# Optimization experiments

Measured on AMD Instinct MI355X. Metric: run time of the kernel, lower is better.

## Reference

```python
import jax, jax.numpy as jnp
import numpy as np

T, A = 4096, 4          # tokens, atoms per token
N = T * A               # flat atoms
QB, KB = 32, 128        # query block / key window (AF3 atom transformer)
S = N // QB             # number of query subsets
H, DK = 4, 32           # heads, key dim per head
NB = 3                  # transformer blocks
CA, CP, CT = 128, 16, 384

# clipped sliding key window centered on each 32-atom query block
KIDX = jnp.clip(jnp.arange(S)[:, None] * QB - (KB - QB) // 2 + jnp.arange(KB)[None, :], 0, N - 1)

PARAM_SHAPES = [('w_ref_pos', (3, CA)), ('w_ref_mask', (1, CA)), ('w_ref_element', (CA, CA)), ('w_ref_charge', (1, CA)), ('w_ref_atom_name', (256, CA)), ('w_s2p_row', (CA, CP)), ('w_s2p_col', (CA, CP)), ('w_pair_offsets', (3, CP)), ('w_pair_dist', (1, CP)), ('w_pair_mask', (1, CP)), ('w_pair_mlp1', (CP, CP)), ('w_pair_mlp2', (CP, CP)), ('w_pair_mlp3', (CP, CP)), ('w_pair_ln', (CP,)), ('w_pair_logits', (CP, NB * H)), ('aq_lnw', (NB, CA)), ('aq_gw', (NB, CA, CA)), ('aq_gb', (NB, CA)), ('aq_sw', (NB, CA, CA)), ('ak_lnw', (NB, CA)), ('ak_gw', (NB, CA, CA)), ('ak_gb', (NB, CA)), ('ak_sw', (NB, CA, CA)), ('wq', (NB, CA, CA)), ('bq', (NB, CA)), ('wk', (NB, CA, CA)), ('wv', (NB, CA, CA)), ('wg', (NB, CA, CA)), ('azi_w', (NB, CA, CA)), ('azi_cw', (NB, CA, CA)), ('azi_cb', (NB, CA)), ('t_lnw', (NB, CA)), ('t_gw', (NB, CA, CA)), ('t_gb', (NB, CA)), ('t_sw', (NB, CA, CA)), ('glu1', (NB, CA, 2 * CA)), ('glu2', (NB, CA, 2 * CA)), ('t_azi_w', (NB, 2 * CA, CA)), ('t_azi_cw', (NB, CA, CA)), ('t_azi_cb', (NB, CA)), ('w_project', (CA, CT))]


def _ln(x, w=None, eps=1e-5):
    mu = jnp.mean(x, -1, keepdims=True)
    var = jnp.var(x, -1, keepdims=True)
    xn = (x - mu) * jax.lax.rsqrt(var + eps)
    return xn * w if w is not None else xn


def _ada_ln(x, cond, lnw, gw, gb, sw):
    c = _ln(cond, lnw)
    return jax.nn.sigmoid(c @ gw + gb) * _ln(x) + c @ sw


def setup_inputs() -> dict:
    ks = iter(jax.random.split(jax.random.key(0), 64))
    d = {}
    d['positions'] = jax.random.normal(next(ks), (T, A, 3), jnp.float32) * 3.0
    d['mask'] = jnp.ones((T, A), jnp.float32)
    d['element'] = jax.random.randint(next(ks), (T, A), 0, 128, jnp.int32)
    d['charge'] = jax.random.normal(next(ks), (T, A), jnp.float32)
    d['atom_name_chars'] = jax.random.randint(next(ks), (T, A, 4), 0, 64, jnp.int32)
    d['ref_space_uid'] = jax.random.randint(next(ks), (T, A), 0, T, jnp.int32)
    for nm, shp in PARAM_SHAPES:
        if nm.endswith('lnw') or nm == 'w_pair_ln':
            d[nm] = jnp.ones(shp, jnp.float32)
        else:
            d[nm] = jax.random.normal(next(ks), shp, jnp.float32) * 0.02
    return d


def _forward(positions, mask, charge, w_ref_pos, w_ref_mask, w_ref_element, w_ref_charge, w_ref_atom_name, w_s2p_row, w_s2p_col, w_pair_offsets, w_pair_dist, w_pair_mask, w_pair_mlp1, w_pair_mlp2, w_pair_mlp3, w_pair_ln, w_pair_logits, aq_lnw, aq_gw, aq_gb, aq_sw, ak_lnw, ak_gw, ak_gb, ak_sw, wq, bq, wk, wv, wg, azi_w, azi_cw, azi_cb, t_lnw, t_gw, t_gb, t_sw, glu1, glu2, t_azi_w, t_azi_cw, t_azi_cb, w_project, element, atom_name_chars, ref_space_uid):
    dt = positions.dtype
    pos = positions.reshape(N, 3)
    m = mask.reshape(N, 1)
    # per_atom_cond
    el1h = jax.nn.one_hot(element.reshape(N), 128, dtype=dt)
    nm1h = jax.nn.one_hot(atom_name_chars.reshape(N, 4), 64, dtype=dt).reshape(N, 256)
    ch = jnp.arcsinh(charge.reshape(N, 1))
    act = pos @ w_ref_pos + m @ w_ref_mask + el1h @ w_ref_element + ch @ w_ref_charge + nm1h @ w_ref_atom_name
    act = act * m
    qsc = act.reshape(S, QB, CA)  # queries_single_cond
    # pair conditioning
    uid = ref_space_uid.reshape(N)
    q_uid, k_uid = uid.reshape(S, QB), uid[KIDX]
    q_pos, k_pos = pos.reshape(S, QB, 3), pos[KIDX]
    valid = (q_uid[:, :, None] == k_uid[:, None, :]).astype(dt)[..., None]  # [S,QB,KB,1]
    off = q_pos[:, :, None, :] - k_pos[:, None, :, :]  # [S,QB,KB,3]
    pair = (off @ w_pair_offsets) * valid
    sq = jnp.sum(off * off, -1, keepdims=True)
    pair = pair + ((1.0 / (1.0 + sq)) @ w_pair_dist) * valid
    ksc = act[KIDX]  # keys_single_cond [S,KB,CA]
    pair = pair + (jax.nn.relu(qsc) @ w_s2p_row)[:, :, None, :] + (jax.nn.relu(ksc) @ w_s2p_col)[:, None, :, :]
    pair = pair + valid @ w_pair_mask
    t = jax.nn.relu(pair) @ w_pair_mlp1
    t = jax.nn.relu(t) @ w_pair_mlp2
    t = jax.nn.relu(t) @ w_pair_mlp3
    pair = pair + t
    # pair logits for all blocks: [NB, S, H, QB, KB]
    pl = (_ln(pair, w_pair_ln) @ w_pair_logits).reshape(S, QB, KB, NB, H)
    pl = jnp.transpose(pl, (3, 0, 4, 1, 2))
    qact = qsc
    scale = DK ** -0.5
    for i in range(NB):
        kact = qact.reshape(N, CA)[KIDX]
        xq = _ada_ln(qact, qsc, aq_lnw[i], aq_gw[i], aq_gb[i], aq_sw[i])
        xk = _ada_ln(kact, ksc, ak_lnw[i], ak_gw[i], ak_gb[i], ak_sw[i])
        q = (xq @ wq[i] + bq[i]).reshape(S, QB, H, DK)
        k = (xk @ wk[i]).reshape(S, KB, H, DK)
        logits = jnp.einsum('sqhd,skhd->shqk', q * scale, k) + pl[i]
        aw = jax.nn.softmax(logits, axis=-1)
        v = (xk @ wv[i]).reshape(S, KB, H, DK)
        o = jnp.einsum('shqk,skhd->sqhd', aw, v).reshape(S, QB, CA)
        o = o * jax.nn.sigmoid(xq @ wg[i])
        o = (o @ azi_w[i]) * jax.nn.sigmoid(qsc @ azi_cw[i] + azi_cb[i])  # AdaptiveZeroInit
        qact = qact + o
        xt = _ada_ln(qact, qsc, t_lnw[i], t_gw[i], t_gb[i], t_sw[i])
        xt = jax.nn.silu(xt @ glu1[i]) * (xt @ glu2[i])  # SwiGLU
        xt = (xt @ t_azi_w[i]) * jax.nn.sigmoid(qsc @ t_azi_cw[i] + t_azi_cb[i])
        qact = qact + xt
    tok = jax.nn.relu(qact.reshape(T, A, CA) @ w_project)
    mm = mask[..., None]
    token_act = jnp.sum(tok * mm, -2) / jnp.maximum(jnp.sum(mm, -2), 1e-10)
    return token_act, qact, qsc, pair


def reference(positions, mask, element, charge, atom_name_chars, ref_space_uid, w_ref_pos, w_ref_mask, w_ref_element, w_ref_charge, w_ref_atom_name, w_s2p_row, w_s2p_col, w_pair_offsets, w_pair_dist, w_pair_mask, w_pair_mlp1, w_pair_mlp2, w_pair_mlp3, w_pair_ln, w_pair_logits, aq_lnw, aq_gw, aq_gb, aq_sw, ak_lnw, ak_gw, ak_gb, ak_sw, wq, bq, wk, wv, wg, azi_w, azi_cw, azi_cb, t_lnw, t_gw, t_gb, t_sw, glu1, glu2, t_azi_w, t_azi_cw, t_azi_cb, w_project):
    return _forward(positions, mask, charge, w_ref_pos, w_ref_mask, w_ref_element, w_ref_charge, w_ref_atom_name, w_s2p_row, w_s2p_col, w_pair_offsets, w_pair_dist, w_pair_mask, w_pair_mlp1, w_pair_mlp2, w_pair_mlp3, w_pair_ln, w_pair_logits, aq_lnw, aq_gw, aq_gb, aq_sw, ak_lnw, ak_gw, ak_gb, ak_sw, wq, bq, wk, wv, wg, azi_w, azi_cw, azi_cb, t_lnw, t_gw, t_gb, t_sw, glu1, glu2, t_azi_w, t_azi_cw, t_azi_cb, w_project, element, atom_name_chars, ref_space_uid)
```

## Files before the change

### kernel.cpp

```cpp
#include <hip/hip_runtime.h>
#include <math.h>

#define TT 4096
#define AA 4
#define NN 16384
#define QBQ 32
#define KBK 128
#define SS 512
#define HH 4
#define DKD 32
#define CAC 128
#define CPC 16
#define CTC 384

typedef __attribute__((ext_vector_type(8))) short bf16x8;
typedef __attribute__((ext_vector_type(4))) short s16x4;
typedef __attribute__((ext_vector_type(4))) float f32x4;

__device__ __forceinline__ float sig_(float x) { return 1.0f / (1.0f + __expf(-x)); }
__device__ __forceinline__ short f2bf(float f) {
    unsigned u = __float_as_uint(f);
    unsigned r = (u + 0x7FFFu + ((u >> 16) & 1u)) >> 16;
    return (short)r;
}
__device__ __forceinline__ float b2f(short s) {
    return __uint_as_float(((unsigned)(unsigned short)s) << 16);
}

struct PEnt { const float* src; const float* rs; short* dst; int K; int NC; };
struct PTab { PEnt e[49]; };

__global__ __launch_bounds__(256) void k_prep(PTab tab)
{
    const PEnt e = tab.e[blockIdx.y];
    const int ntx = e.NC >> 5, nty = e.K >> 5, nt = ntx * nty;
    __shared__ float sm[32][33];
    const int lx = threadIdx.x & 31, ly = threadIdx.x >> 5;
    for (int t = blockIdx.x; t < nt; t += gridDim.x) {
        const int ty = t / ntx, tx = t - ty * ntx;
        #pragma unroll
        for (int j = 0; j < 4; ++j) {
            const int k = ty * 32 + ly + j * 8;
            const int n = tx * 32 + lx;
            float v = e.src[(size_t)k * e.NC + n];
            if (e.rs) v *= e.rs[k];
            sm[ly + j * 8][lx] = v;
        }
        __syncthreads();
        #pragma unroll
        for (int j = 0; j < 4; ++j) {
            const int n = tx * 32 + ly + j * 8;
            const int k = ty * 32 + lx;
            e.dst[(size_t)n * e.K + k] = f2bf(sm[lx][ly + j * 8]);
        }
        __syncthreads();
    }
}

__global__ __launch_bounds__(128) void k_atom_cond(
    const float* __restrict__ pos, const float* __restrict__ msk,
    const int* __restrict__ elem, const float* __restrict__ chg,
    const int* __restrict__ chars,
    const float* __restrict__ w_pos, const float* __restrict__ w_msk,
    const float* __restrict__ w_elem, const float* __restrict__ w_chg,
    const float* __restrict__ w_name,
    const float* __restrict__ w_row, const float* __restrict__ w_col,
    float* __restrict__ qsc, float* __restrict__ qact,
    short* __restrict__ qsc_bf, short* __restrict__ qn_bf,
    float* __restrict__ stats,
    float* __restrict__ rq, float* __restrict__ rk)
{
    const int n = blockIdx.x, c = threadIdx.x;
    const float p0 = pos[n*3+0], p1 = pos[n*3+1], p2 = pos[n*3+2];
    const float m = msk[n];
    const int   el = elem[n];
    const float ach = asinhf(chg[n]);
    const int c0 = chars[n*4+0], c1 = chars[n*4+1], c2 = chars[n*4+2], c3 = chars[n*4+3];

    float a = p0*w_pos[c] + p1*w_pos[CAC+c] + p2*w_pos[2*CAC+c]
            + m*w_msk[c] + w_elem[el*CAC+c] + ach*w_chg[c]
            + w_name[(c0      )*CAC+c] + w_name[( 64+c1)*CAC+c]
            + w_name[(128+c2)*CAC+c] + w_name[(192+c3)*CAC+c];
    a *= m;

    const size_t base = (size_t)n*CAC + c;
    qsc[base] = a; qact[base] = a; qsc_bf[base] = f2bf(a);

    __shared__ float red[128];
    __shared__ float sh[128];
    red[c] = a; __syncthreads();
    for (int off = 64; off > 0; off >>= 1) { if (c < off) red[c] += red[c+off]; __syncthreads(); }
    const float mu = red[0] * (1.0f/128.0f);
    __syncthreads();
    const float d = a - mu;
    red[c] = d*d; __syncthreads();
    for (int off = 64; off > 0; off >>= 1) { if (c < off) red[c] += red[c+off]; __syncthreads(); }
    const float var = red[0] * (1.0f/128.0f);
    const float rs = rsqrtf(var + 1e-5f);
    qn_bf[base] = f2bf(d * rs);
    if (c == 0) { stats[2*n] = mu; stats[2*n+1] = rs; }
    __syncthreads();
    sh[c] = fmaxf(a, 0.0f);
    __syncthreads();
    if (c < 32) {
        const float* w = (c < 16) ? w_row : w_col;
        const int cc = c & 15;
        float acc = 0.0f;
        #pragma unroll 8
        for (int r = 0; r < 128; ++r) acc += sh[r] * w[r*CPC + cc];
        if (c < 16) rq[(size_t)n*CPC + cc] = acc;
        else        rk[(size_t)n*CPC + cc] = acc;
    }
}

__global__ __launch_bounds__(256) void k_pair(
    const float* __restrict__ pos, const int* __restrict__ uid,
    const float* __restrict__ rq, const float* __restrict__ rk,
    const float* __restrict__ w_ofs, const float* __restrict__ w_dist,
    const float* __restrict__ w_pm,
    const float* __restrict__ mlp1, const float* __restrict__ mlp2,
    const float* __restrict__ mlp3,
    const float* __restrict__ wln, const float* __restrict__ wpl,
    float* __restrict__ pair, short* __restrict__ plb)
{
    __shared__ float sm1[256], sm2[256], sm3[256], sofs[48], sdist[16], smask[16];
    __shared__ float swln[16], swpl[192];
    const int tid = threadIdx.x;
    sm1[tid] = mlp1[tid]; sm2[tid] = mlp2[tid]; sm3[tid] = mlp3[tid];
    if (tid < 48) sofs[tid] = w_ofs[tid];
    if (tid < 16) { sdist[tid] = w_dist[tid]; smask[tid] = w_pm[tid]; swln[tid] = wln[tid]; }
    if (tid < 192) swpl[tid] = wpl[tid];
    __syncthreads();

    const int gid = blockIdx.x*256 + tid;
    const int s = gid >> 12;
    const int rem = gid & 4095;
    const int q = rem >> 7, kk = rem & 127;
    const int n = s*QBQ + q;
    int kidx = s*QBQ - 48 + kk; kidx = max(0, min(NN-1, kidx));

    const float v = (uid[n] == uid[kidx]) ? 1.0f : 0.0f;
    const float o0 = pos[n*3+0]-pos[kidx*3+0];
    const float o1 = pos[n*3+1]-pos[kidx*3+1];
    const float o2 = pos[n*3+2]-pos[kidx*3+2];
    const float sq = o0*o0 + o1*o1 + o2*o2;
    const float inv = 1.0f/(1.0f + sq);

    const float* rqp = rq + (size_t)n*CPC;
    const float* rkp = rk + (size_t)kidx*CPC;

    float p[16], t1[16], t2[16];
    #pragma unroll
    for (int j = 0; j < 16; ++j)
        p[j] = v*(o0*sofs[j] + o1*sofs[16+j] + o2*sofs[32+j] + inv*sdist[j] + smask[j])
             + rqp[j] + rkp[j];
    #pragma unroll
    for (int j = 0; j < 16; ++j) {
        float acc = 0.0f;
        #pragma unroll
        for (int r = 0; r < 16; ++r) acc += fmaxf(p[r], 0.0f) * sm1[r*16+j];
        t1[j] = acc;
    }
    #pragma unroll
    for (int j = 0; j < 16; ++j) {
        float acc = 0.0f;
        #pragma unroll
        for (int r = 0; r < 16; ++r) acc += fmaxf(t1[r], 0.0f) * sm2[r*16+j];
        t2[j] = acc;
    }
    #pragma unroll
    for (int j = 0; j < 16; ++j) {
        float acc = 0.0f;
        #pragma unroll
        for (int r = 0; r < 16; ++r) acc += fmaxf(t2[r], 0.0f) * sm3[r*16+j];
        t1[j] = p[j] + acc;
    }
    float* op = pair + (size_t)gid*CPC;
    #pragma unroll
    for (int j = 0; j < 4; ++j)
        *(float4*)(op + j*4) = make_float4(t1[j*4], t1[j*4+1], t1[j*4+2], t1[j*4+3]);

    float sm = 0.0f;
    #pragma unroll
    for (int j = 0; j < 16; ++j) sm += t1[j];
    const float mu = sm * (1.0f/16.0f);
    float vq = 0.0f;
    #pragma unroll
    for (int j = 0; j < 16; ++j) { const float dd = t1[j]-mu; vq += dd*dd; }
    const float rs = rsqrtf(vq*(1.0f/16.0f) + 1e-5f);
    float xn[16];
    #pragma unroll
    for (int j = 0; j < 16; ++j) xn[j] = (t1[j]-mu)*rs*swln[j];
    #pragma unroll
    for (int i = 0; i < 3; ++i) {
        #pragma unroll
        for (int h = 0; h < 4; ++h) {
            float acc = 0.0f;
            #pragma unroll
            for (int j = 0; j < 16; ++j) acc += xn[j] * swpl[j*12 + i*4 + h];
            plb[((((size_t)i*SS + s)*HH + h)*QBQ + q)*KBK + kk] = f2bf(acc);
        }
    }
}

struct FJob {
    const void* A; const void* A2;
    const float* stats; const short* G; const short* S;
    const short* Bt; const float* bias;
    float* outF; short* outB;
    const short* gate; float* resid; float* ostats;
    int K; int ostride; int amode; int emode;
};
struct FJobs { FJob j[8]; };

__global__ __launch_bounds__(256) void k_mmf(FJobs jobs)
{
    __shared__ short As[128*64];
    __shared__ short Bs[128*64];
    const FJob J = jobs.j[blockIdx.y];
    const int tid = threadIdx.x;
    const int wave = tid >> 6, lane = tid & 63;
    const int l15 = lane & 15, l4 = lane >> 4;
    const int row0 = blockIdx.x * 128;
    const int K = J.K;

    f32x4 acc[2][8];
    #pragma unroll
    for (int m = 0; m < 2; ++m)
        #pragma unroll
        for (int n = 0; n < 8; ++n) acc[m][n] = (f32x4){0.f,0.f,0.f,0.f};

    for (int k0 = 0; k0 < K; k0 += 64) {
        #pragma unroll
        for (int j = 0; j < 4; ++j) {
            const int u = tid + j*256;
            const int r = u >> 3, ug = u & 7;
            const int row = row0 + r;
            const size_t ao = (size_t)row*K + k0 + ug*8;
            bf16x8 av;
            if (J.amode == 0) {
                av = *(const bf16x8*)((const short*)J.A + ao);
            } else if (J.amode == 1) {
                const float* Af = (const float*)J.A;
                const float4 a0 = *(const float4*)(Af + ao);
                const float4 a1 = *(const float4*)(Af + ao + 4);
                const float mu = J.stats[2*row], rs = J.stats[2*row+1];
                const s16x4 g0 = *(const s16x4*)(J.G + ao), g1 = *(const s16x4*)(J.G + ao + 4);
                const s16x4 s0 = *(const s16x4*)(J.S + ao), s1 = *(const s16x4*)(J.S + ao + 4);
                const float x[8] = {a0.x,a0.y,a0.z,a0.w,a1.x,a1.y,a1.z,a1.w};
                #pragma unroll
                for (int t = 0; t < 4; ++t) {
                    av[t]   = f2bf(b2f(g0[t])*((x[t]  -mu)*rs) + b2f(s0[t]));
                    av[t+4] = f2bf(b2f(g1[t])*((x[t+4]-mu)*rs) + b2f(s1[t]));
                }
            } else if (J.amode == 2) {
                const float* Ao = (const float*)J.A;
                const float* Ag = (const float*)J.A2;
                const float4 oa = *(const float4*)(Ao + ao);
                const float4 ob = *(const float4*)(Ao + ao + 4);
                const float4 ga = *(const float4*)(Ag + ao);
                const float4 gb = *(const float4*)(Ag + ao + 4);
                av[0]=f2bf(oa.x*ga.x); av[1]=f2bf(oa.y*ga.y); av[2]=f2bf(oa.z*ga.z); av[3]=f2bf(oa.w*ga.w);
                av[4]=f2bf(ob.x*gb.x); av[5]=f2bf(ob.y*gb.y); av[6]=f2bf(ob.z*gb.z); av[7]=f2bf(ob.w*gb.w);
            } else {
                const float* Af = (const float*)J.A;
                const float4 a0 = *(const float4*)(Af + ao);
                const float4 a1 = *(const float4*)(Af + ao + 4);
                av[0]=f2bf(a0.x); av[1]=f2bf(a0.y); av[2]=f2bf(a0.z); av[3]=f2bf(a0.w);
                av[4]=f2bf(a1.x); av[5]=f2bf(a1.y); av[6]=f2bf(a1.z); av[7]=f2bf(a1.w);
            }
            *(bf16x8*)&As[r*64 + ((ug ^ (r & 7)) * 8)] = av;
            const bf16x8 bv = *(const bf16x8*)(J.Bt + (size_t)r*K + k0 + ug*8);
            *(bf16x8*)&Bs[r*64 + ((ug ^ (r & 7)) * 8)] = bv;
        }
        __syncthreads();
        #pragma unroll
        for (int ks = 0; ks < 2; ++ks) {
            bf16x8 af[2], bfr[8];
            #pragma unroll
            for (int m = 0; m < 2; ++m) {
                const int r = wave*32 + m*16 + l15;
                af[m] = *(const bf16x8*)&As[r*64 + (((ks*4 + l4) ^ (r & 7)) * 8)];
            }
            #pragma unroll
            for (int n = 0; n < 8; ++n) {
                const int c = n*16 + l15;
                bfr[n] = *(const bf16x8*)&Bs[c*64 + (((ks*4 + l4) ^ (c & 7)) * 8)];
            }
            #pragma unroll
            for (int m = 0; m < 2; ++m)
                #pragma unroll
                for (int n = 0; n < 8; ++n)
                    acc[m][n] = __builtin_amdgcn_mfma_f32_16x16x32_bf16(af[m], bfr[n], acc[m][n], 0, 0, 0);
        }
        __syncthreads();
    }

    if (J.emode == 3) {
        #pragma unroll
        for (int m = 0; m < 2; ++m) {
            #pragma unroll
            for (int reg = 0; reg < 4; ++reg) {
                const int row = row0 + wave*32 + m*16 + l4*4 + reg;
                float s = 0.0f, q = 0.0f;
                #pragma unroll
                for (int n = 0; n < 8; ++n) {
                    const int col = n*16 + l15;
                    const size_t off = (size_t)row*CAC + col;
                    const float v = J.resid[off] + acc[m][n][reg] * b2f(J.gate[off]);
                    J.resid[off] = v;
                    s += v; q += v*v;
                }
                #pragma unroll
                for (int msk = 1; msk < 16; msk <<= 1) {
                    s += __shfl_xor(s, msk, 64);
                    q += __shfl_xor(q, msk, 64);
                }
                if (l15 == 0) {
                    const float mu = s * (1.0f/128.0f);
                    const float var = q * (1.0f/128.0f) - mu*mu;
                    J.ostats[2*row]   = mu;
                    J.ostats[2*row+1] = rsqrtf(var + 1e-5f);
                }
            }
        }
    } else {
        float bval[8];
        #pragma unroll
        for (int n = 0; n < 8; ++n) bval[n] = 0.0f;
        if (J.bias) {
            #pragma unroll
            for (int n = 0; n < 8; ++n) bval[n] = J.bias[n*16 + l15];
        }
        const int epi = J.emode;
        #pragma unroll
        for (int m = 0; m < 2; ++m) {
            #pragma unroll
            for (int n = 0; n < 8; ++n) {
                const int col = n*16 + l15;
                #pragma unroll
                for (int reg = 0; reg < 4; ++reg) {
                    const int row = row0 + wave*32 + m*16 + l4*4 + reg;
                    float v = acc[m][n][reg] + bval[n];
                    if (epi == 1) v = sig_(v);
                    if (epi == 2) v = fmaxf(v, 0.0f);
                    if (J.outB) J.outB[(size_t)row*J.ostride + col] = f2bf(v);
                    else        J.outF[(size_t)row*J.ostride + col] = v;
                }
            }
        }
    }
}

__global__ __launch_bounds__(256) void k_mm_glu(
    const float* __restrict__ qact, const float* __restrict__ stats,
    const short* __restrict__ Gt, const short* __restrict__ St,
    const short* __restrict__ B1t, const short* __restrict__ B2t,
    short* __restrict__ out)
{
    __shared__ short As[128*64];
    __shared__ short B1s[64*64];
    __shared__ short B2s[64*64];
    const int tid = threadIdx.x;
    const int wave = tid >> 6, lane = tid & 63;
    const int l15 = lane & 15, l4 = lane >> 4;
    const int row0 = blockIdx.x * 128;
    const int col0 = blockIdx.y * 64;

    f32x4 acc1[2][4], acc2[2][4];
    #pragma unroll
    for (int m = 0; m < 2; ++m)
        #pragma unroll
        for (int n = 0; n < 4; ++n) {
            acc1[m][n] = (f32x4){0.f,0.f,0.f,0.f};
            acc2[m][n] = (f32x4){0.f,0.f,0.f,0.f};
        }

    for (int k0 = 0; k0 < 128; k0 += 64) {
        #pragma unroll
        for (int j = 0; j < 4; ++j) {
            const int u = tid + j*256;
            const int r = u >> 3, ug = u & 7;
            const int row = row0 + r;
            const size_t ao = (size_t)row*CAC + k0 + ug*8;
            const float4 a0 = *(const float4*)(qact + ao);
            const float4 a1 = *(const float4*)(qact + ao + 4);
            const float mu = stats[2*row], rs = stats[2*row+1];
            const s16x4 g0 = *(const s16x4*)(Gt + ao), g1 = *(const s16x4*)(Gt + ao + 4);
            const s16x4 s0 = *(const s16x4*)(St + ao), s1 = *(const s16x4*)(St + ao + 4);
            const float x[8] = {a0.x,a0.y,a0.z,a0.w,a1.x,a1.y,a1.z,a1.w};
            bf16x8 av;
            #pragma unroll
            for (int t = 0; t < 4; ++t) {
                av[t]   = f2bf(b2f(g0[t])*((x[t]  -mu)*rs) + b2f(s0[t]));
                av[t+4] = f2bf(b2f(g1[t])*((x[t+4]-mu)*rs) + b2f(s1[t]));
            }
            *(bf16x8*)&As[r*64 + ((ug ^ (r & 7)) * 8)] = av;
        }
        #pragma unroll
        for (int j = 0; j < 2; ++j) {
            const int u = tid + j*256;
            const int r = u >> 3, ug = u & 7;
            const bf16x8 b1 = *(const bf16x8*)(B1t + (size_t)(col0 + r)*128 + k0 + ug*8);
            *(bf16x8*)&B1s[r*64 + ((ug ^ (r & 7)) * 8)] = b1;
            const bf16x8 b2 = *(const bf16x8*)(B2t + (size_t)(col0 + r)*128 + k0 + ug*8);
            *(bf16x8*)&B2s[r*64 + ((ug ^ (r & 7)) * 8)] = b2;
        }
        __syncthreads();
        #pragma unroll
        for (int ks = 0; ks < 2; ++ks) {
            bf16x8 af[2], bq1[4], bq2[4];
            #pragma unroll
            for (int m = 0; m < 2; ++m) {
                const int r = wave*32 + m*16 + l15;
                af[m] = *(const bf16x8*)&As[r*64 + (((ks*4 + l4) ^ (r & 7)) * 8)];
            }
            #pragma unroll
            for (int n = 0; n < 4; ++n) {
                const int c = n*16 + l15;
                bq1[n] = *(const bf16x8*)&B1s[c*64 + (((ks*4 + l4) ^ (c & 7)) * 8)];
                bq2[n] = *(const bf16x8*)&B2s[c*64 + (((ks*4 + l4) ^ (c & 7)) * 8)];
            }
            #pragma unroll
            for (int m = 0; m < 2; ++m)
                #pragma unroll
                for (int n = 0; n < 4; ++n) {
                    acc1[m][n] = __builtin_amdgcn_mfma_f32_16x16x32_bf16(af[m], bq1[n], acc1[m][n], 0, 0, 0);
                    acc2[m][n] = __builtin_amdgcn_mfma_f32_16x16x32_bf16(af[m], bq2[n], acc2[m][n], 0, 0, 0);
                }
        }
        __syncthreads();
    }

    #pragma unroll
    for (int m = 0; m < 2; ++m)
        #pragma unroll
        for (int n = 0; n < 4; ++n) {
            const int col = col0 + n*16 + l15;
            #pragma unroll
            for (int reg = 0; reg < 4; ++reg) {
                const int row = row0 + wave*32 + m*16 + l4*4 + reg;
                const float a1 = acc1[m][n][reg];
                const float h = a1 * sig_(a1) * acc2[m][n][reg];
                out[(size_t)row*256 + col] = f2bf(h);
            }
        }
}

__global__ __launch_bounds__(512) void k_attn2(
    const float* __restrict__ qh, const float* __restrict__ kh,
    const float* __restrict__ vh, const short* __restrict__ pls,
    float* __restrict__ oh)
{
    __shared__ float sm_m[256], sm_l[256], sm_acc[256*17];
    const int s = blockIdx.x, tid = threadIdx.x;
    const int kh2 = tid >> 8;
    const int h = (tid >> 6) & 3;
    const int q = (tid >> 1) & 31;
    const int dh = tid & 1;
    const int n0 = s*QBQ;
    const int kbase = n0 - 48 + kh2*64;
    const float SCALE = 0.17677669529663687f;

    float qr[32];
    {
        const float* qp = qh + (size_t)(n0+q)*CAC + h*DKD;
        #pragma unroll
        for (int j = 0; j < 8; ++j) {
            const float4 v4 = *(const float4*)(qp + j*4);
            qr[j*4]=v4.x*SCALE; qr[j*4+1]=v4.y*SCALE; qr[j*4+2]=v4.z*SCALE; qr[j*4+3]=v4.w*SCALE;
        }
    }
    const short* plp = pls + (((size_t)s*HH + h)*QBQ + q)*KBK + kh2*64;

    float m = -1e30f, l = 0.0f;
    float acc[16];
    #pragma unroll
    for (int j = 0; j < 16; ++j) acc[j] = 0.0f;

    for (int kb4 = 0; kb4 < 16; ++kb4) {
        const s16x4 p4 = *(const s16x4*)(plp + kb4*4);
        float pv[4];
        #pragma unroll
        for (int j = 0; j < 4; ++j) pv[j] = b2f(p4[j]);
        #pragma unroll
        for (int j = 0; j < 4; ++j) {
            const int kb = kb4*4 + j;
            int kidx = kbase + kb; kidx = max(0, min(NN-1, kidx));
            const float* kp = kh + (size_t)kidx*CAC + h*DKD;
            float dot = 0.0f;
            #pragma unroll
            for (int jj = 0; jj < 8; ++jj) {
                const float4 kv = *(const float4*)(kp + jj*4);
                dot += qr[jj*4]*kv.x + qr[jj*4+1]*kv.y + qr[jj*4+2]*kv.z + qr[jj*4+3]*kv.w;
            }
            const float sv = dot + pv[j];
            if (sv > m) {
                const float corr = __expf(m - sv);
                l *= corr;
                #pragma unroll
                for (int d = 0; d < 16; ++d) acc[d] *= corr;
                m = sv;
            }
            const float w = __expf(sv - m);
            l += w;
            const float* vp = vh + (size_t)kidx*CAC + h*DKD + dh*16;
            #pragma unroll
            for (int jj = 0; jj < 4; ++jj) {
                const float4 vv = *(const float4*)(vp + jj*4);
                acc[jj*4]   = fmaf(w, vv.x, acc[jj*4]);
                acc[jj*4+1] = fmaf(w, vv.y, acc[jj*4+1]);
                acc[jj*4+2] = fmaf(w, vv.z, acc[jj*4+2]);
                acc[jj*4+3] = fmaf(w, vv.w, acc[jj*4+3]);
            }
        }
    }

    const int part = tid & 255;
    if (kh2 == 1) {
        sm_m[part] = m; sm_l[part] = l;
        #pragma unroll
        for (int j = 0; j < 16; ++j) sm_acc[part*17 + j] = acc[j];
    }
    __syncthreads();
    if (kh2 == 0) {
        const float m2 = sm_m[part], l2 = sm_l[part];
        const float mm = fmaxf(m, m2);
        const float c1 = __expf(m - mm), c2 = __expf(m2 - mm);
        const float inv = 1.0f / (l*c1 + l2*c2);
        float* op = oh + (size_t)(n0+q)*CAC + h*DKD + dh*16;
        #pragma unroll
        for (int jj = 0; jj < 4; ++jj) {
            float o0 = (acc[jj*4  ]*c1 + sm_acc[part*17+jj*4  ]*c2) * inv;
            float o1 = (acc[jj*4+1]*c1 + sm_acc[part*17+jj*4+1]*c2) * inv;
            float o2 = (acc[jj*4+2]*c1 + sm_acc[part*17+jj*4+2]*c2) * inv;
            float o3 = (acc[jj*4+3]*c1 + sm_acc[part*17+jj*4+3]*c2) * inv;
            *(float4*)op = make_float4(o0,o1,o2,o3);
            op += 4;
        }
    }
}

__global__ __launch_bounds__(256) void k_token_reduce(
    const float* __restrict__ tok, const float* __restrict__ msk, float* __restrict__ out)
{
    const int gid = blockIdx.x*256 + threadIdx.x;
    const int t = gid / CTC, c = gid - t*CTC;
    float num = 0.0f, den = 0.0f;
    #pragma unroll
    for (int a = 0; a < AA; ++a) {
        const float mv = msk[t*AA + a];
        num += tok[(size_t)(t*AA+a)*CTC + c] * mv;
        den += mv;
    }
    out[gid] = num / fmaxf(den, 1e-10f);
}

static inline FJob fj0() { FJob j{}; return j; }

extern "C" void kernel_launch(void* const* d_in, const int* in_sizes, int n_in,
                              void* d_out, int out_size, void* d_ws, size_t ws_size,
                              hipStream_t stream)
{
    const float* positions = (const float*)d_in[0];
    const float* maskp     = (const float*)d_in[1];
    const int*   element   = (const int*  )d_in[2];
    const float* charge    = (const float*)d_in[3];
    const int*   chars     = (const int*  )d_in[4];
    const int*   uid       = (const int*  )d_in[5];
    const float* w_ref_pos      = (const float*)d_in[6];
    const float* w_ref_mask     = (const float*)d_in[7];
    const float* w_ref_element  = (const float*)d_in[8];
    const float* w_ref_charge   = (const float*)d_in[9];
    const float* w_ref_atom_name= (const float*)d_in[10];
    const float* w_s2p_row      = (const float*)d_in[11];
    const float* w_s2p_col      = (const float*)d_in[12];
    const float* w_pair_offsets = (const float*)d_in[13];
    const float* w_pair_dist    = (const float*)d_in[14];
    const float* w_pair_mask    = (const float*)d_in[15];
    const float* w_pair_mlp1    = (const float*)d_in[16];
    const float* w_pair_mlp2    = (const float*)d_in[17];
    const float* w_pair_mlp3    = (const float*)d_in[18];
    const float* w_pair_ln      = (const float*)d_in[19];
    const float* w_pair_logits  = (const float*)d_in[20];
    const float* aq_lnw = (const float*)d_in[21];
    const float* aq_gw  = (const float*)d_in[22];
    const float* aq_gb  = (const float*)d_in[23];
    const float* aq_sw  = (const float*)d_in[24];
    const float* ak_lnw = (const float*)d_in[25];
    const float* ak_gw  = (const float*)d_in[26];
    const float* ak_gb  = (const float*)d_in[27];
    const float* ak_sw  = (const float*)d_in[28];
    const float* wq     = (const float*)d_in[29];
    const float* bq     = (const float*)d_in[30];
    const float* wk     = (const float*)d_in[31];
    const float* wv     = (const float*)d_in[32];
    const float* wg     = (const float*)d_in[33];
    const float* azi_w  = (const float*)d_in[34];
    const float* azi_cw = (const float*)d_in[35];
    const float* azi_cb = (const float*)d_in[36];
    const float* t_lnw  = (const float*)d_in[37];
    const float* t_gw   = (const float*)d_in[38];
    const float* t_gb   = (const float*)d_in[39];
    const float* t_sw   = (const float*)d_in[40];
    const float* glu1   = (const float*)d_in[41];
    const float* glu2   = (const float*)d_in[42];
    const float* t_azi_w  = (const float*)d_in[43];
    const float* t_azi_cw = (const float*)d_in[44];
    const float* t_azi_cb = (const float*)d_in[45];
    const float* w_project= (const float*)d_in[46];

    float* token_o = (float*)d_out;
    float* qact = token_o + 1572864;
    float* qsc  = token_o + 3670016;
    float* pair = token_o + 5767168;

    char* W = (char*)d_ws;
    short* pl_bf   = (short*)(W);
    short* wbf     = (short*)(W + 50331648);
    short* qn_bf   = (short*)(W + 52428800);
    short* qsc_bf  = (short*)(W + 56623104);
    float* stats   = (float*)(W + 60817408);
    short* Gq_bf   = (short*)(W + 60948480);
    short* Sq_bf   = (short*)(W + 65142784);
    short* Gk_bf   = (short*)(W + 69337088);
    short* Sk_bf   = (short*)(W + 73531392);
    short* Gt_bf   = (short*)(W + 77725696);
    short* St_bf   = (short*)(W + 81920000);
    short* Ag_bf   = (short*)(W + 86114304);
    short* Tg_bf   = (short*)(W + 90308608);
    float* w_q     = (float*)(W + 94502912);
    float* w_k     = (float*)(W + 102891520);
    float* w_v     = (float*)(W + 111280128);
    float* w_g     = (float*)(W + 119668736);
    float* w_o     = (float*)(W + 128057344);
    short* hs_bf   = (short*)(W + 136445952);
    float* rq      = (float*)(W + 144834560);
    float* rk      = (float*)(W + 145883136);
    float* tok = w_q;

    (void)in_sizes; (void)n_in; (void)out_size; (void)ws_size;

    const size_t LSTR = 311296;
    const size_t oGQ=0, oSQ=16384, oGK=32768, oSK=49152, oGT=65536, oST=81920,
                 oWQ=98304, oWK=114688, oWV=131072, oWG=147456, oAZ=163840,
                 oACW=180224, oTCW=196608, oG1=212992, oG2=245760, oTAW=278528;
    const size_t oPROJ = 3*LSTR;

    {
        PTab tab{};
        int e = 0;
        for (int i = 0; i < 3; ++i) {
            short* L = wbf + (size_t)i*LSTR;
            const size_t oM = (size_t)i*CAC*CAC, oV = (size_t)i*CAC, oGL = (size_t)i*CAC*2*CAC;
            tab.e[e++] = {aq_gw+oM,  aq_lnw+oV, L+oGQ,  128, 128};
            tab.e[e++] = {aq_sw+oM,  aq_lnw+oV, L+oSQ,  128, 128};
            tab.e[e++] = {ak_gw+oM,  ak_lnw+oV, L+oGK,  128, 128};
            tab.e[e++] = {ak_sw+oM,  ak_lnw+oV, L+oSK,  128, 128};
            tab.e[e++] = {t_gw+oM,   t_lnw+oV,  L+oGT,  128, 128};
            tab.e[e++] = {t_sw+oM,   t_lnw+oV,  L+oST,  128, 128};
            tab.e[e++] = {wq+oM,     nullptr,   L+oWQ,  128, 128};
            tab.e[e++] = {wk+oM,     nullptr,   L+oWK,  128, 128};
            tab.e[e++] = {wv+oM,     nullptr,   L+oWV,  128, 128};
            tab.e[e++] = {wg+oM,     nullptr,   L+oWG,  128, 128};
            tab.e[e++] = {azi_w+oM,  nullptr,   L+oAZ,  128, 128};
            tab.e[e++] = {azi_cw+oM, nullptr,   L+oACW, 128, 128};
            tab.e[e++] = {t_azi_cw+oM,nullptr,  L+oTCW, 128, 128};
            tab.e[e++] = {glu1+oGL,  nullptr,   L+oG1,  128, 256};
            tab.e[e++] = {glu2+oGL,  nullptr,   L+oG2,  128, 256};
            tab.e[e++] = {t_azi_w+oGL,nullptr,  L+oTAW, 256, 128};
        }
        tab.e[e++] = {w_project, nullptr, wbf+oPROJ, 128, 384};
        k_prep<<<dim3(48, 49), 256, 0, stream>>>(tab);
    }

    k_atom_cond<<<NN, 128, 0, stream>>>(positions, maskp, element, charge, chars,
        w_ref_pos, w_ref_mask, w_ref_element, w_ref_charge, w_ref_atom_name,
        w_s2p_row, w_s2p_col, qsc, qact, qsc_bf, qn_bf, stats, rq, rk);

    k_pair<<<(SS*QBQ*KBK)/256, 256, 0, stream>>>(positions, uid, rq, rk,
        w_pair_offsets, w_pair_dist, w_pair_mask, w_pair_mlp1, w_pair_mlp2, w_pair_mlp3,
        w_pair_ln, w_pair_logits, pair, pl_bf);

    for (int i = 0; i < 3; ++i) {
        short* L = wbf + (size_t)i*LSTR;
        const size_t oV = (size_t)i*CAC;

        {
            FJobs js{};
            struct { const short* A; const short* Bt; const float* bias; short* out; int em; } cfg[8] = {
                {qn_bf,  L+oGQ,  aq_gb+oV,    Gq_bf, 1}, {qn_bf,  L+oSQ,  nullptr, Sq_bf, 0},
                {qn_bf,  L+oGK,  ak_gb+oV,    Gk_bf, 1}, {qn_bf,  L+oSK,  nullptr, Sk_bf, 0},
                {qn_bf,  L+oGT,  t_gb+oV,     Gt_bf, 1}, {qn_bf,  L+oST,  nullptr, St_bf, 0},
                {qsc_bf, L+oACW, azi_cb+oV,   Ag_bf, 1}, {qsc_bf, L+oTCW, t_azi_cb+oV, Tg_bf, 1}};
            for (int jn = 0; jn < 8; ++jn) {
                FJob j = fj0();
                j.A = cfg[jn].A; j.Bt = cfg[jn].Bt; j.bias = cfg[jn].bias;
                j.outB = cfg[jn].out; j.K = 128; j.ostride = 128;
                j.amode = 0; j.emode = cfg[jn].em;
                js.j[jn] = j;
            }
            k_mmf<<<dim3(128, 8), 256, 0, stream>>>(js);
        }
        {
            FJobs js{};
            struct { const short* G; const short* S; const short* Bt; const float* bias; float* out; int em; } cfg[4] = {
                {Gq_bf, Sq_bf, L+oWQ, bq+oV,   w_q, 0}, {Gk_bf, Sk_bf, L+oWK, nullptr, w_k, 0},
                {Gk_bf, Sk_bf, L+oWV, nullptr, w_v, 0}, {Gq_bf, Sq_bf, L+oWG, nullptr, w_g, 1}};
            for (int jn = 0; jn < 4; ++jn) {
                FJob j = fj0();
                j.A = qact; j.stats = stats; j.G = cfg[jn].G; j.S = cfg[jn].S;
                j.Bt = cfg[jn].Bt; j.bias = cfg[jn].bias; j.outF = cfg[jn].out;
                j.K = 128; j.ostride = 128; j.amode = 1; j.emode = cfg[jn].em;
                js.j[jn] = j;
            }
            k_mmf<<<dim3(128, 4), 256, 0, stream>>>(js);
        }
        k_attn2<<<SS, 512, 0, stream>>>(w_q, w_k, w_v, pl_bf + (size_t)i*8388608, w_o);
        {
            FJobs js{};
            FJob j = fj0();
            j.A = w_o; j.A2 = w_g; j.Bt = L+oAZ;
            j.gate = Ag_bf; j.resid = qact; j.ostats = stats;
            j.K = 128; j.ostride = 128; j.amode = 2; j.emode = 3;
            js.j[0] = j;
            k_mmf<<<dim3(128, 1), 256, 0, stream>>>(js);
        }
        k_mm_glu<<<dim3(128, 4), 256, 0, stream>>>(qact, stats, Gt_bf, St_bf, L+oG1, L+oG2, hs_bf);
        {
            FJobs js{};
            FJob j = fj0();
            j.A = hs_bf; j.Bt = L+oTAW;
            j.gate = Tg_bf; j.resid = qact; j.ostats = stats;
            j.K = 256; j.ostride = 128; j.amode = 0; j.emode = 3;
            js.j[0] = j;
            k_mmf<<<dim3(128, 1), 256, 0, stream>>>(js);
        }
    }

    {
        FJobs js{};
        for (int c = 0; c < 3; ++c) {
            FJob j = fj0();
            j.A = qact; j.Bt = wbf + oPROJ + (size_t)c*16384;
            j.outF = tok + c*128;
            j.K = 128; j.ostride = 384; j.amode = 3; j.emode = 2;
            js.j[c] = j;
        }
        k_mmf<<<dim3(128, 3), 256, 0, stream>>>(js);
    }
    k_token_reduce<<<(TT*CTC)/256, 256, 0, stream>>>(tok, maskp, token_o);
}
```

Before: 933.9 us.

## Halve GEMM row tiles to 64 and fuse token mask-reduce into projection epilogue

Templates the fused GEMM kernel on the M-tile so each block covers 64 rows instead of 128, and does the same for the GLU kernel. With 16384 rows this doubles the grid to 256 blocks per job, raising occupancy and CU coverage, but each B tile is now loaded twice as often. Separately, the final projection epilogue applies ReLU and the masked mean over the 4 atoms of each token directly from the accumulators. This removes the intermediate token buffer and the separate reduce kernel launch.

```diff
diff --git a/kernel.cpp b/kernel.cpp
--- a/kernel.cpp
+++ b/kernel.cpp
@@ -209,30 +209,32 @@
     const short* Bt; const float* bias;
     float* outF; short* outB;
     const short* gate; float* resid; float* ostats;
+    const float* msk;
     int K; int ostride; int amode; int emode;
 };
 struct FJobs { FJob j[8]; };
 
+template<int MF>
 __global__ __launch_bounds__(256) void k_mmf(FJobs jobs)
 {
-    __shared__ short As[128*64];
+    __shared__ short As[MF*64*64];
     __shared__ short Bs[128*64];
     const FJob J = jobs.j[blockIdx.y];
     const int tid = threadIdx.x;
     const int wave = tid >> 6, lane = tid & 63;
     const int l15 = lane & 15, l4 = lane >> 4;
-    const int row0 = blockIdx.x * 128;
+    const int row0 = blockIdx.x * (MF*64);
     const int K = J.K;
 
-    f32x4 acc[2][8];
-    #pragma unroll
-    for (int m = 0; m < 2; ++m)
+    f32x4 acc[MF][8];
+    #pragma unroll
+    for (int m = 0; m < MF; ++m)
         #pragma unroll
         for (int n = 0; n < 8; ++n) acc[m][n] = (f32x4){0.f,0.f,0.f,0.f};
 
     for (int k0 = 0; k0 < K; k0 += 64) {
         #pragma unroll
-        for (int j = 0; j < 4; ++j) {
+        for (int j = 0; j < MF*2; ++j) {
             const int u = tid + j*256;
             const int r = u >> 3, ug = u & 7;
             const int row = row0 + r;
@@ -244,14 +246,14 @@
                 const float* Af = (const float*)J.A;
                 const float4 a0 = *(const float4*)(Af + ao);
                 const float4 a1 = *(const float4*)(Af + ao + 4);
-                const float mu = J.stats[2*row], rs = J.stats[2*row+1];
+                const float mu = J.stats[2*row], rsd = J.stats[2*row+1];
                 const s16x4 g0 = *(const s16x4*)(J.G + ao), g1 = *(const s16x4*)(J.G + ao + 4);
                 const s16x4 s0 = *(const s16x4*)(J.S + ao), s1 = *(const s16x4*)(J.S + ao + 4);
                 const float x[8] = {a0.x,a0.y,a0.z,a0.w,a1.x,a1.y,a1.z,a1.w};
                 #pragma unroll
                 for (int t = 0; t < 4; ++t) {
-                    av[t]   = f2bf(b2f(g0[t])*((x[t]  -mu)*rs) + b2f(s0[t]));
-                    av[t+4] = f2bf(b2f(g1[t])*((x[t+4]-mu)*rs) + b2f(s1[t]));
+                    av[t]   = f2bf(b2f(g0[t])*((x[t]  -mu)*rsd) + b2f(s0[t]));
+                    av[t+4] = f2bf(b2f(g1[t])*((x[t+4]-mu)*rsd) + b2f(s1[t]));
                 }
             } else if (J.amode == 2) {
                 const float* Ao = (const float*)J.A;
@@ -270,16 +272,21 @@
                 av[4]=f2bf(a1.x); av[5]=f2bf(a1.y); av[6]=f2bf(a1.z); av[7]=f2bf(a1.w);
             }
             *(bf16x8*)&As[r*64 + ((ug ^ (r & 7)) * 8)] = av;
-            const bf16x8 bv = *(const bf16x8*)(J.Bt + (size_t)r*K + k0 + ug*8);
-            *(bf16x8*)&Bs[r*64 + ((ug ^ (r & 7)) * 8)] = bv;
+        }
+        #pragma unroll
+        for (int j = 0; j < 4; ++j) {
+            const int u = tid + j*256;
+            const int r = u >> 3, ug = u & 7;
+            *(bf16x8*)&Bs[r*64 + ((ug ^ (r & 7)) * 8)] =
+                *(const bf16x8*)(J.Bt + (size_t)r*K + k0 + ug*8);
         }
         __syncthreads();
         #pragma unroll
         for (int ks = 0; ks < 2; ++ks) {
-            bf16x8 af[2], bfr[8];
-            #pragma unroll
-            for (int m = 0; m < 2; ++m) {
-                const int r = wave*32 + m*16 + l15;
+            bf16x8 af[MF], bfr[8];
+            #pragma unroll
+            for (int m = 0; m < MF; ++m) {
+                const int r = wave*(16*MF) + m*16 + l15;
                 af[m] = *(const bf16x8*)&As[r*64 + (((ks*4 + l4) ^ (r & 7)) * 8)];
             }
             #pragma unroll
@@ -288,7 +295,7 @@
                 bfr[n] = *(const bf16x8*)&Bs[c*64 + (((ks*4 + l4) ^ (c & 7)) * 8)];
             }
             #pragma unroll
-            for (int m = 0; m < 2; ++m)
+            for (int m = 0; m < MF; ++m)
                 #pragma unroll
                 for (int n = 0; n < 8; ++n)
                     acc[m][n] = __builtin_amdgcn_mfma_f32_16x16x32_bf16(af[m], bfr[n], acc[m][n], 0, 0, 0);
@@ -298,10 +305,10 @@
 
     if (J.emode == 3) {
         #pragma unroll
-        for (int m = 0; m < 2; ++m) {
+        for (int m = 0; m < MF; ++m) {
             #pragma unroll
             for (int reg = 0; reg < 4; ++reg) {
-                const int row = row0 + wave*32 + m*16 + l4*4 + reg;
+                const int row = row0 + wave*(16*MF) + m*16 + l4*4 + reg;
                 float s = 0.0f, q = 0.0f;
                 #pragma unroll
                 for (int n = 0; n < 8; ++n) {
@@ -312,9 +319,9 @@
                     s += v; q += v*v;
                 }
                 #pragma unroll
-                for (int msk = 1; msk < 16; msk <<= 1) {
-                    s += __shfl_xor(s, msk, 64);
-                    q += __shfl_xor(q, msk, 64);
+                for (int msk_ = 1; msk_ < 16; msk_ <<= 1) {
+                    s += __shfl_xor(s, msk_, 64);
+                    q += __shfl_xor(q, msk_, 64);
                 }
                 if (l15 == 0) {
                     const float mu = s * (1.0f/128.0f);
@@ -324,6 +331,24 @@
                 }
             }
         }
+    } else if (J.emode == 4) {
+        #pragma unroll
+        for (int m = 0; m < MF; ++m) {
+            const int rbase = row0 + wave*(16*MF) + m*16 + l4*4;
+            const int t = rbase >> 2;
+            const float4 mv = *(const float4*)(J.msk + (size_t)rbase);
+            const float den = fmaxf(mv.x + mv.y + mv.z + mv.w, 1e-10f);
+            const float inv = 1.0f / den;
+            #pragma unroll
+            for (int n = 0; n < 8; ++n) {
+                const int col = n*16 + l15;
+                const float num = fmaxf(acc[m][n][0], 0.f)*mv.x
+                                + fmaxf(acc[m][n][1], 0.f)*mv.y
+                                + fmaxf(acc[m][n][2], 0.f)*mv.z
+                                + fmaxf(acc[m][n][3], 0.f)*mv.w;
+                J.outF[(size_t)t*J.ostride + col] = num * inv;
+            }
+        }
     } else {
         float bval[8];
         #pragma unroll
@@ -334,13 +359,13 @@
         }
         const int epi = J.emode;
         #pragma unroll
-        for (int m = 0; m < 2; ++m) {
+        for (int m = 0; m < MF; ++m) {
             #pragma unroll
             for (int n = 0; n < 8; ++n) {
                 const int col = n*16 + l15;
                 #pragma unroll
                 for (int reg = 0; reg < 4; ++reg) {
-                    const int row = row0 + wave*32 + m*16 + l4*4 + reg;
+                    const int row = row0 + wave*(16*MF) + m*16 + l4*4 + reg;
                     float v = acc[m][n][reg] + bval[n];
                     if (epi == 1) v = sig_(v);
                     if (epi == 2) v = fmaxf(v, 0.0f);
@@ -358,93 +383,81 @@
     const short* __restrict__ B1t, const short* __restrict__ B2t,
     short* __restrict__ out)
 {
-    __shared__ short As[128*64];
+    __shared__ short As[64*64];
     __shared__ short B1s[64*64];
     __shared__ short B2s[64*64];
     const int tid = threadIdx.x;
     const int wave = tid >> 6, lane = tid & 63;
     const int l15 = lane & 15, l4 = lane >> 4;
-    const int row0 = blockIdx.x * 128;
+    const int row0 = blockIdx.x * 64;
     const int col0 = blockIdx.y * 64;
 
-    f32x4 acc1[2][4], acc2[2][4];
-    #pragma unroll
-    for (int m = 0; m < 2; ++m)
-        #pragma unroll
-        for (int n = 0; n < 4; ++n) {
-            acc1[m][n] = (f32x4){0.f,0.f,0.f,0.f};
-            acc2[m][n] = (f32x4){0.f,0.f,0.f,0.f};
-        }
+    f32x4 acc1[4], acc2[4];
+    #pragma unroll
+    for (int n = 0; n < 4; ++n) {
+        acc1[n] = (f32x4){0.f,0.f,0.f,0.f};
+        acc2[n] = (f32x4){0.f,0.f,0.f,0.f};
+    }
 
     for (int k0 = 0; k0 < 128; k0 += 64) {
         #pragma unroll
-        for (int j = 0; j < 4; ++j) {
+        for (int j = 0; j < 2; ++j) {
             const int u = tid + j*256;
             const int r = u >> 3, ug = u & 7;
             const int row = row0 + r;
             const size_t ao = (size_t)row*CAC + k0 + ug*8;
             const float4 a0 = *(const float4*)(qact + ao);
             const float4 a1 = *(const float4*)(qact + ao + 4);
-            const float mu = stats[2*row], rs = stats[2*row+1];
+            const float mu = stats[2*row], rsd = stats[2*row+1];
             const s16x4 g0 = *(const s16x4*)(Gt + ao), g1 = *(const s16x4*)(Gt + ao + 4);
             const s16x4 s0 = *(const s16x4*)(St + ao), s1 = *(const s16x4*)(St + ao + 4);
             const float x[8] = {a0.x,a0.y,a0.z,a0.w,a1.x,a1.y,a1.z,a1.w};
             bf16x8 av;
             #pragma unroll
             for (int t = 0; t < 4; ++t) {
-                av[t]   = f2bf(b2f(g0[t])*((x[t]  -mu)*rs) + b2f(s0[t]));
-                av[t+4] = f2bf(b2f(g1[t])*((x[t+4]-mu)*rs) + b2f(s1[t]));
-            }
-            *(bf16x8*)&As[r*64 + ((ug ^ (r & 7)) * 8)] = av;
-        }
-        #pragma unroll
-        for (int j = 0; j < 2; ++j) {
-            const int u = tid + j*256;
-            const int r = u >> 3, ug = u & 7;
-            const bf16x8 b1 = *(const bf16x8*)(B1t + (size_t)(col0 + r)*128 + k0 + ug*8);
-            *(bf16x8*)&B1s[r*64 + ((ug ^ (r & 7)) * 8)] = b1;
-            const bf16x8 b2 = *(const bf16x8*)(B2t + (size_t)(col0 + r)*128 + k0 + ug*8);
-            *(bf16x8*)&B2s[r*64 + ((ug ^ (r & 7)) * 8)] = b2;
+                av[t]   = f2bf(b2f(g0[t])*((x[t]  -mu)*rsd) + b2f(s0[t]));
+                av[t+4] = f2bf(b2f(g1[t])*((x[t+4]-mu)*rsd) + b2f(s1[t]));
+            }
+            const int sw = (ug ^ (r & 7)) * 8;
+            *(bf16x8*)&As[r*64 + sw] = av;
+            const size_t bo = (size_t)(col0 + r)*CAC + k0 + ug*8;
+            *(bf16x8*)&B1s[r*64 + sw] = *(const bf16x8*)(B1t + bo);
+            *(bf16x8*)&B2s[r*64 + sw] = *(const bf16x8*)(B2t + bo);
         }
         __syncthreads();
         #pragma unroll
         for (int ks = 0; ks < 2; ++ks) {
-            bf16x8 af[2], bq1[4], bq2[4];
-            #pragma unroll
-            for (int m = 0; m < 2; ++m) {
-                const int r = wave*32 + m*16 + l15;
-                af[m] = *(const bf16x8*)&As[r*64 + (((ks*4 + l4) ^ (r & 7)) * 8)];
+            bf16x8 af, b1f[4], b2f_[4];
+            {
+                const int r = wave*16 + l15;
+                af = *(const bf16x8*)&As[r*64 + (((ks*4 + l4) ^ (r & 7)) * 8)];
             }
             #pragma unroll
             for (int n = 0; n < 4; ++n) {
                 const int c = n*16 + l15;
-                bq1[n] = *(const bf16x8*)&B1s[c*64 + (((ks*4 + l4) ^ (c & 7)) * 8)];
-                bq2[n] = *(const bf16x8*)&B2s[c*64 + (((ks*4 + l4) ^ (c & 7)) * 8)];
-            }
-            #pragma unroll
-            for (int m = 0; m < 2; ++m)
-                #pragma unroll
-                for (int n = 0; n < 4; ++n) {
-                    acc1[m][n] = __builtin_amdgcn_mfma_f32_16x16x32_bf16(af[m], bq1[n], acc1[m][n], 0, 0, 0);
-                    acc2[m][n] = __builtin_amdgcn_mfma_f32_16x16x32_bf16(af[m], bq2[n], acc2[m][n], 0, 0, 0);
-                }
+                const int sw = ((ks*4 + l4) ^ (c & 7)) * 8;
+                b1f[n] = *(const bf16x8*)&B1s[c*64 + sw];
+                b2f_[n] = *(const bf16x8*)&B2s[c*64 + sw];
+            }
+            #pragma unroll
+            for (int n = 0; n < 4; ++n) {
+                acc1[n] = __builtin_amdgcn_mfma_f32_16x16x32_bf16(af, b1f[n], acc1[n], 0, 0, 0);
+                acc2[n] = __builtin_amdgcn_mfma_f32_16x16x32_bf16(af, b2f_[n], acc2[n], 0, 0, 0);
+            }
         }
         __syncthreads();
     }
 
     #pragma unroll
-    for (int m = 0; m < 2; ++m)
-        #pragma unroll
-        for (int n = 0; n < 4; ++n) {
-            const int col = col0 + n*16 + l15;
-            #pragma unroll
-            for (int reg = 0; reg < 4; ++reg) {
-                const int row = row0 + wave*32 + m*16 + l4*4 + reg;
-                const float a1 = acc1[m][n][reg];
-                const float h = a1 * sig_(a1) * acc2[m][n][reg];
-                out[(size_t)row*256 + col] = f2bf(h);
-            }
-        }
+    for (int n = 0; n < 4; ++n) {
+        const int col = col0 + n*16 + l15;
+        #pragma unroll
+        for (int reg = 0; reg < 4; ++reg) {
+            const int row = row0 + wave*16 + l4*4 + reg;
+            const float a1 = acc1[n][reg];
+            out[(size_t)row*256 + col] = f2bf(a1 * sig_(a1) * acc2[n][reg]);
+        }
+    }
 }
 
 __global__ __launch_bounds__(512) void k_attn2(
@@ -539,21 +552,6 @@
             op += 4;
         }
     }
-}
-
-__global__ __launch_bounds__(256) void k_token_reduce(
-    const float* __restrict__ tok, const float* __restrict__ msk, float* __restrict__ out)
-{
-    const int gid = blockIdx.x*256 + threadIdx.x;
-    const int t = gid / CTC, c = gid - t*CTC;
-    float num = 0.0f, den = 0.0f;
-    #pragma unroll
-    for (int a = 0; a < AA; ++a) {
-        const float mv = msk[t*AA + a];
-        num += tok[(size_t)(t*AA+a)*CTC + c] * mv;
-        den += mv;
-    }
-    out[gid] = num / fmaxf(den, 1e-10f);
 }
 
 static inline FJob fj0() { FJob j{}; return j; }
@@ -637,7 +635,6 @@
     short* hs_bf   = (short*)(W + 136445952);
     float* rq      = (float*)(W + 144834560);
     float* rk      = (float*)(W + 145883136);
-    float* tok = w_q;
 
     (void)in_sizes; (void)n_in; (void)out_size; (void)ws_size;
 
@@ -700,7 +697,7 @@
                 j.amode = 0; j.emode = cfg[jn].em;
                 js.j[jn] = j;
             }
-            k_mmf<<<dim3(128, 8), 256, 0, stream>>>(js);
+            k_mmf<1><<<dim3(256, 8), 256, 0, stream>>>(js);
         }
         {
             FJobs js{};
@@ -714,7 +711,7 @@
                 j.K = 128; j.ostride = 128; j.amode = 1; j.emode = cfg[jn].em;
                 js.j[jn] = j;
             }
-            k_mmf<<<dim3(128, 4), 256, 0, stream>>>(js);
+            k_mmf<1><<<dim3(256, 4), 256, 0, stream>>>(js);
         }
         k_attn2<<<SS, 512, 0, stream>>>(w_q, w_k, w_v, pl_bf + (size_t)i*8388608, w_o);
         {
@@ -724,9 +721,9 @@
             j.gate = Ag_bf; j.resid = qact; j.ostats = stats;
             j.K = 128; j.ostride = 128; j.amode = 2; j.emode = 3;
             js.j[0] = j;
-            k_mmf<<<dim3(128, 1), 256, 0, stream>>>(js);
-        }
-        k_mm_glu<<<dim3(128, 4), 256, 0, stream>>>(qact, stats, Gt_bf, St_bf, L+oG1, L+oG2, hs_bf);
+            k_mmf<1><<<dim3(256, 1), 256, 0, stream>>>(js);
+        }
+        k_mm_glu<<<dim3(256, 4), 256, 0, stream>>>(qact, stats, Gt_bf, St_bf, L+oG1, L+oG2, hs_bf);
         {
             FJobs js{};
             FJob j = fj0();
@@ -734,7 +731,7 @@
             j.gate = Tg_bf; j.resid = qact; j.ostats = stats;
             j.K = 256; j.ostride = 128; j.amode = 0; j.emode = 3;
             js.j[0] = j;
-            k_mmf<<<dim3(128, 1), 256, 0, stream>>>(js);
+            k_mmf<1><<<dim3(256, 1), 256, 0, stream>>>(js);
         }
     }
 
@@ -743,11 +740,10 @@
         for (int c = 0; c < 3; ++c) {
             FJob j = fj0();
             j.A = qact; j.Bt = wbf + oPROJ + (size_t)c*16384;
-            j.outF = tok + c*128;
-            j.K = 128; j.ostride = 384; j.amode = 3; j.emode = 2;
+            j.outF = token_o + c*128; j.msk = maskp;
+            j.K = 128; j.ostride = CTC; j.amode = 3; j.emode = 4;
             js.j[c] = j;
         }
-        k_mmf<<<dim3(128, 3), 256, 0, stream>>>(js);
-    }
-    k_token_reduce<<<(TT*CTC)/256, 256, 0, stream>>>(tok, maskp, token_o);
-}
+        k_mmf<1><<<dim3(256, 3), 256, 0, stream>>>(js);
+    }
+}
```

Result: faster. 851.3 us (-8.8%).
